# Kernel optimization log

Hardware: AMD Instinct MI355X
Metric: run time of the kernel (lower is better)

Reference implementation:

```python
import math
import jax, jax.numpy as jnp
import numpy as np

B, M, L, H = 8, 2048, 2048, 1024


def setup_inputs() -> dict:
    key = jax.random.key(0)
    k1, k2, k3, k4 = jax.random.split(key, 4)
    return {
        "query": jax.random.normal(k1, (B, M, H), dtype=jnp.float32),
        "key": jax.random.normal(k2, (B, L, H), dtype=jnp.float32),
        "value": jax.random.normal(k3, (B, L, H), dtype=jnp.float32),
        "key_pe": jax.random.normal(k4, (1, H, L), dtype=jnp.float32),
        "hidden_size": H,
    }


def reference(query, key, value, key_pe, hidden_size):
    # content scores: [B, M, L]
    attn_cont = jnp.einsum("bmh,blh->bml", query, key)
    # relative-position scores: [B, M, H] @ [1, H, L] -> [B, M, L]
    attn_pos = jnp.matmul(query, key_pe)
    # NOTE: the original module computes softmax(attn)+dropout but then
    # (as written) multiplies VALUE by the raw content scores, not the
    # softmaxed attention. We reproduce that math faithfully; the softmax
    # is dead code w.r.t. the output (kept here for documentation, DCE'd by jit).
    attn = jax.nn.softmax((attn_cont + attn_pos) / math.sqrt(hidden_size), axis=-1)  # noqa: F841
    # dropout: identity in eval mode (and unused for the output anyway)
    out = jnp.matmul(attn_cont, value)  # [B, M, H]
    return out
```

## Files before the change

kernel.cpp:

```cpp
#include <hip/hip_runtime.h>
#include <hip/hip_bf16.h>


typedef __bf16 bf16x8 __attribute__((ext_vector_type(8)));
typedef float f32x4 __attribute__((ext_vector_type(4)));
typedef unsigned short u16_t;

#define GLD_LDS16(g, l)                                                        \
  __builtin_amdgcn_global_load_lds(                                            \
      (const __attribute__((address_space(1))) void*)(g),                      \
      (__attribute__((address_space(3))) void*)(l), 16, 0, 0)

static __device__ inline u16_t f2b(float x) {
  __hip_bfloat16 h = __float2bfloat16(x);
  u16_t u;
  __builtin_memcpy(&u, &h, 2);
  return u;
}
static __device__ inline unsigned pack2(float a, float b) {
  return (unsigned)f2b(a) | ((unsigned)f2b(b) << 16);
}
static __device__ inline float b2f(u16_t u) {
  unsigned v = (unsigned)u << 16;
  float f;
  __builtin_memcpy(&f, &v, 4);
  return f;
}

__global__ __launch_bounds__(256) void transpose_kv(
    const float* __restrict__ Kin, const float* __restrict__ Vin,
    u16_t* __restrict__ Kt, u16_t* __restrict__ Vt, int L, int Hd, int ldT) {
  __shared__ unsigned tile[64][260];
  const int bz = blockIdx.z;
  const float* in = (bz < 8) ? Kin : Vin;
  u16_t* out = (bz < 8) ? Kt : Vt;
  const int batch = bz & 7;
  in += (size_t)batch * (size_t)L * Hd;
  out += (size_t)batch * (size_t)Hd * ldT;
  const int h0 = blockIdx.x * 64;
  const int l0 = blockIdx.y * 512;

  const int tid = threadIdx.x;
  const int h4 = (tid & 15) * 4;
  const int lp0 = tid >> 4;

#pragma unroll
  for (int g = 0; g < 4; ++g) {
    float4 r0[4], r1[4];
#pragma unroll
    for (int it = 0; it < 4; ++it) {
      const int lp = lp0 + 16 * (4 * g + it);
      const int l = l0 + 2 * lp;
      r0[it] = *(const float4*)(in + (size_t)l * Hd + h0 + h4);
      r1[it] = *(const float4*)(in + (size_t)(l + 1) * Hd + h0 + h4);
    }
#pragma unroll
    for (int it = 0; it < 4; ++it) {
      const int lp = lp0 + 16 * (4 * g + it);
      tile[h4 + 0][lp] = pack2(r0[it].x, r1[it].x);
      tile[h4 + 1][lp] = pack2(r0[it].y, r1[it].y);
      tile[h4 + 2][lp] = pack2(r0[it].z, r1[it].z);
      tile[h4 + 3][lp] = pack2(r0[it].w, r1[it].w);
    }
  }
  __syncthreads();

  const int wv = tid >> 6;
  const int lane = tid & 63;
#pragma unroll
  for (int r = 0; r < 16; ++r) {
    const int h = wv * 16 + r;
    unsigned u[4];
#pragma unroll
    for (int j = 0; j < 4; ++j) u[j] = tile[h][4 * lane + j];
    *(uint4*)(out + (size_t)(h0 + h) * ldT + l0 + lane * 8) = *(const uint4*)u;
  }
}

static __device__ inline void store_c(float* p, float v) { *p = v; }
static __device__ inline void store_c(u16_t* p, float v) { *p = f2b(v); }

template <typename OutT>
static __device__ inline void gemm_bt_body(
    const u16_t* __restrict__ A, const u16_t* __restrict__ Bt,
    OutT* __restrict__ C, int N, int K, int ldA, int ldB,
    long sA, long sB, long sC, int tile_shift, long sCsplit) {
  __shared__ __align__(16) u16_t As[128 * 64];
  __shared__ __align__(16) u16_t Bs[128 * 64];

  const int batch = blockIdx.x & 7;
  const unsigned u = blockIdx.x >> 3;
  const int kh = (int)(u >> tile_shift);
  const unsigned t = u & ((1u << tile_shift) - 1u);
  const int m0 = (int)(t >> 3) * 128;
  const int n0 = (int)(t & 7) * 128;

  A  += (size_t)batch * (size_t)sA + (size_t)kh * (size_t)K;
  Bt += (size_t)batch * (size_t)sB + (size_t)kh * (size_t)K;
  C  += (size_t)batch * (size_t)sC + (size_t)kh * (size_t)sCsplit;

  const int tid = threadIdx.x;
  const int lane = tid & 63;
  const int w  = tid >> 6;
  const int wm = w & 1;
  const int wn = w >> 1;
  const int s  = lane & 15;
  const int q  = lane >> 4;

  const u16_t* gA[4];
  const u16_t* gB[4];
  u16_t* lA[4];
  u16_t* lB[4];
#pragma unroll
  for (int j = 0; j < 4; ++j) {
    const int i = tid + 256 * j;
    const int row = i >> 3;
    const int gchunk = (i & 7) ^ (row & 7);
    gA[j] = A  + (size_t)(m0 + row) * ldA + gchunk * 8;
    gB[j] = Bt + (size_t)(n0 + row) * ldB + gchunk * 8;
    lA[j] = As + i * 8;
    lB[j] = Bs + i * 8;
  }

  f32x4 acc[4][4];
#pragma unroll
  for (int r = 0; r < 4; ++r)
#pragma unroll
    for (int c = 0; c < 4; ++c) acc[r][c] = (f32x4){0.f, 0.f, 0.f, 0.f};

  const int s7 = s & 7;

  for (int k0 = 0; k0 < K; k0 += 64) {
#pragma unroll
    for (int j = 0; j < 4; ++j) {
      GLD_LDS16(gA[j] + k0, lA[j]);
      GLD_LDS16(gB[j] + k0, lB[j]);
    }
    __syncthreads();

#pragma unroll
    for (int kk = 0; kk < 2; ++kk) {
      const int slot = (kk * 4 + q) ^ s7;
      bf16x8 af[4], bfr[4];
#pragma unroll
      for (int r = 0; r < 4; ++r)
        af[r] = *(const bf16x8*)(As + (64 * wm + 16 * r + s) * 64 + slot * 8);
#pragma unroll
      for (int c = 0; c < 4; ++c)
        bfr[c] = *(const bf16x8*)(Bs + (64 * wn + 16 * c + s) * 64 + slot * 8);
#pragma unroll
      for (int r = 0; r < 4; ++r)
#pragma unroll
        for (int c = 0; c < 4; ++c)
          acc[r][c] = __builtin_amdgcn_mfma_f32_16x16x32_bf16(af[r], bfr[c],
                                                              acc[r][c], 0, 0, 0);
    }
    __syncthreads();
  }

#pragma unroll
  for (int r = 0; r < 4; ++r) {
#pragma unroll
    for (int c = 0; c < 4; ++c) {
      const int col = n0 + 64 * wn + 16 * c + s;
#pragma unroll
      for (int e = 0; e < 4; ++e) {
        const int row = m0 + 64 * wm + 16 * r + q * 4 + e;
        store_c(&C[(size_t)row * N + col], acc[r][c][e]);
      }
    }
  }
}

__global__ __launch_bounds__(256) void gemm1_kv(
    const u16_t* __restrict__ Vt, const u16_t* __restrict__ Kt,
    u16_t* __restrict__ W0, int N, int K, int ld, long sA, long sB, long sC,
    long sCsplit) {
  gemm_bt_body<u16_t>(Vt, Kt, W0, N, K, ld, ld, sA, sB, sC, 6, sCsplit);
}

__global__ __launch_bounds__(256) void gemm2_qw(
    const u16_t* __restrict__ Qb, const u16_t* __restrict__ Wb,
    float* __restrict__ C, int N, int K, long sA, long sB, long sC) {
  gemm_bt_body<float>(Qb, Wb, C, N, K, K, K, sA, sB, sC, 7, 0);
}

__global__ __launch_bounds__(256) void qcvt_wsum(
    const float* __restrict__ Q, const u16_t* __restrict__ W0,
    const u16_t* __restrict__ W1, u16_t* __restrict__ Qb,
    u16_t* __restrict__ Wb, size_t nQbatch, size_t nWbatch) {
  const int batch = blockIdx.y;
  if (blockIdx.z == 0) {
    const size_t base = (size_t)batch * nWbatch +
                        (size_t)blockIdx.x * 2048 + threadIdx.x * 8;
    const uint4 u0 = *(const uint4*)(W0 + base);
    const uint4 u1 = *(const uint4*)(W1 + base);
    const u16_t* p0 = (const u16_t*)&u0;
    const u16_t* p1 = (const u16_t*)&u1;
    u16_t o[8];
#pragma unroll
    for (int j = 0; j < 8; ++j) o[j] = f2b(b2f(p0[j]) + b2f(p1[j]));
    *(uint4*)(Wb + base) = *(const uint4*)o;
  } else {
    const size_t base = (size_t)batch * nQbatch +
                        (size_t)blockIdx.x * 4096 + threadIdx.x * 16;
    const float* src = Q + base;
    u16_t* dst = Qb + base;
#pragma unroll
    for (int half = 0; half < 2; ++half) {
      const float4 a = *(const float4*)(src + half * 8);
      const float4 b = *(const float4*)(src + half * 8 + 4);
      unsigned o[4] = {pack2(a.x, a.y), pack2(a.z, a.w),
                       pack2(b.x, b.y), pack2(b.z, b.w)};
      *(uint4*)(dst + half * 8) = *(const uint4*)o;
    }
  }
}

extern "C" void kernel_launch(void* const* d_in, const int* in_sizes, int n_in,
                              void* d_out, int out_size, void* d_ws, size_t ws_size,
                              hipStream_t stream) {
  const int B = 8, M = 2048, L = 2048, H = 1024;
  const int ldT = L + 16;

  const float* q = (const float*)d_in[0];
  const float* k = (const float*)d_in[1];
  const float* v = (const float*)d_in[2];

  const size_t nKtP = (size_t)B * H * ldT;
  const size_t nW   = (size_t)B * H * H;
  const size_t nQ   = (size_t)B * M * H;
  const size_t need = (2 * nKtP + 2 * nW) * sizeof(u16_t);
  if (ws_size < need) return;

  u16_t* Kt = (u16_t*)d_ws;
  u16_t* Vt = Kt + nKtP;
  u16_t* W0 = Vt + nKtP;
  u16_t* W1 = W0 + nW;
  u16_t* Qb = Kt;
  u16_t* Wb = Vt;
  (void)nQ;

  dim3 tb(256);

  transpose_kv<<<dim3(H / 64, L / 512, 16), tb, 0, stream>>>(k, v, Kt, Vt, L, H,
                                                             ldT);

  gemm1_kv<<<dim3(B * 64 * 2), tb, 0, stream>>>(
      Vt, Kt, W0, H, L / 2, ldT, (long)H * ldT, (long)H * ldT, (long)H * H,
      (long)B * H * H);

  qcvt_wsum<<<dim3(512, B, 2), tb, 0, stream>>>(
      q, W0, W1, Qb, Wb, (size_t)M * H, (size_t)H * H);

  gemm2_qw<<<dim3(B * 128), tb, 0, stream>>>(
      Qb, Wb, (float*)d_out, H, H, (long)M * H, (long)H * H, (long)M * H);
}
```

Before: 330.4 us.

## Enlarge GEMM tiles to 256x256 with 512 threads and double-buffered LDS

Result: faster. 308.9 us (-6.5%).

```diff
diff --git a/kernel.cpp b/kernel.cpp
--- a/kernel.cpp
+++ b/kernel.cpp
@@ -81,19 +81,19 @@
 static __device__ inline void store_c(u16_t* p, float v) { *p = f2b(v); }
 
 template <typename OutT>
-static __device__ inline void gemm_bt_body(
+static __device__ inline void gemm256_body(
     const u16_t* __restrict__ A, const u16_t* __restrict__ Bt,
     OutT* __restrict__ C, int N, int K, int ldA, int ldB,
     long sA, long sB, long sC, int tile_shift, long sCsplit) {
-  __shared__ __align__(16) u16_t As[128 * 64];
-  __shared__ __align__(16) u16_t Bs[128 * 64];
+  __shared__ __align__(16) u16_t As[2][256 * 64];
+  __shared__ __align__(16) u16_t Bs[2][256 * 64];
 
   const int batch = blockIdx.x & 7;
   const unsigned u = blockIdx.x >> 3;
   const int kh = (int)(u >> tile_shift);
   const unsigned t = u & ((1u << tile_shift) - 1u);
-  const int m0 = (int)(t >> 3) * 128;
-  const int n0 = (int)(t & 7) * 128;
+  const int m0 = (int)(t >> 2) * 256;
+  const int n0 = (int)(t & 3) * 256;
 
   A  += (size_t)batch * (size_t)sA + (size_t)kh * (size_t)K;
   Bt += (size_t)batch * (size_t)sB + (size_t)kh * (size_t)K;
@@ -106,83 +106,91 @@
   const int wn = w >> 1;
   const int s  = lane & 15;
   const int q  = lane >> 4;
+  const int s7 = s & 7;
 
   const u16_t* gA[4];
   const u16_t* gB[4];
-  u16_t* lA[4];
-  u16_t* lB[4];
+  int lofs[4];
 #pragma unroll
   for (int j = 0; j < 4; ++j) {
-    const int i = tid + 256 * j;
+    const int i = tid + 512 * j;
     const int row = i >> 3;
     const int gchunk = (i & 7) ^ (row & 7);
     gA[j] = A  + (size_t)(m0 + row) * ldA + gchunk * 8;
     gB[j] = Bt + (size_t)(n0 + row) * ldB + gchunk * 8;
-    lA[j] = As + i * 8;
-    lB[j] = Bs + i * 8;
-  }
-
-  f32x4 acc[4][4];
-#pragma unroll
-  for (int r = 0; r < 4; ++r)
+    lofs[j] = i * 8;
+  }
+
+  f32x4 acc[8][4];
+#pragma unroll
+  for (int r = 0; r < 8; ++r)
 #pragma unroll
     for (int c = 0; c < 4; ++c) acc[r][c] = (f32x4){0.f, 0.f, 0.f, 0.f};
 
-  const int s7 = s & 7;
-
-  for (int k0 = 0; k0 < K; k0 += 64) {
-#pragma unroll
-    for (int j = 0; j < 4; ++j) {
-      GLD_LDS16(gA[j] + k0, lA[j]);
-      GLD_LDS16(gB[j] + k0, lB[j]);
-    }
-    __syncthreads();
-
+  auto STAGE = [&](u16_t* dA, u16_t* dB, int k0) {
+#pragma unroll
+    for (int j = 0; j < 4; ++j) GLD_LDS16(gA[j] + k0, dA + lofs[j]);
+#pragma unroll
+    for (int j = 0; j < 4; ++j) GLD_LDS16(gB[j] + k0, dB + lofs[j]);
+  };
+
+  auto COMPUTE = [&](const u16_t* As_, const u16_t* Bs_) {
 #pragma unroll
     for (int kk = 0; kk < 2; ++kk) {
       const int slot = (kk * 4 + q) ^ s7;
-      bf16x8 af[4], bfr[4];
-#pragma unroll
-      for (int r = 0; r < 4; ++r)
-        af[r] = *(const bf16x8*)(As + (64 * wm + 16 * r + s) * 64 + slot * 8);
+      bf16x8 bfr[4];
 #pragma unroll
       for (int c = 0; c < 4; ++c)
-        bfr[c] = *(const bf16x8*)(Bs + (64 * wn + 16 * c + s) * 64 + slot * 8);
-#pragma unroll
-      for (int r = 0; r < 4; ++r)
+        bfr[c] = *(const bf16x8*)(Bs_ + (64 * wn + 16 * c + s) * 64 + slot * 8);
+#pragma unroll
+      for (int r = 0; r < 8; ++r) {
+        const bf16x8 af =
+            *(const bf16x8*)(As_ + (128 * wm + 16 * r + s) * 64 + slot * 8);
 #pragma unroll
         for (int c = 0; c < 4; ++c)
-          acc[r][c] = __builtin_amdgcn_mfma_f32_16x16x32_bf16(af[r], bfr[c],
+          acc[r][c] = __builtin_amdgcn_mfma_f32_16x16x32_bf16(af, bfr[c],
                                                               acc[r][c], 0, 0, 0);
-    }
+      }
+    }
+  };
+
+  const int nt = K / 64;
+  STAGE(As[0], Bs[0], 0);
+  __syncthreads();
+  for (int tt = 0; tt < nt; tt += 2) {
+    if (tt + 1 < nt) STAGE(As[1], Bs[1], (tt + 1) * 64);
+    COMPUTE(As[0], Bs[0]);
     __syncthreads();
-  }
-
-#pragma unroll
-  for (int r = 0; r < 4; ++r) {
+    if (tt + 2 < nt) STAGE(As[0], Bs[0], (tt + 2) * 64);
+    COMPUTE(As[1], Bs[1]);
+    __syncthreads();
+  }
+
+#pragma unroll
+  for (int r = 0; r < 8; ++r) {
 #pragma unroll
     for (int c = 0; c < 4; ++c) {
       const int col = n0 + 64 * wn + 16 * c + s;
 #pragma unroll
       for (int e = 0; e < 4; ++e) {
-        const int row = m0 + 64 * wm + 16 * r + q * 4 + e;
+        const int row = m0 + 128 * wm + 16 * r + q * 4 + e;
         store_c(&C[(size_t)row * N + col], acc[r][c][e]);
       }
     }
   }
 }
 
-__global__ __launch_bounds__(256) void gemm1_kv(
+__global__ __launch_bounds__(512) void gemm1_kv(
     const u16_t* __restrict__ Vt, const u16_t* __restrict__ Kt,
     u16_t* __restrict__ W0, int N, int K, int ld, long sA, long sB, long sC,
     long sCsplit) {
-  gemm_bt_body<u16_t>(Vt, Kt, W0, N, K, ld, ld, sA, sB, sC, 6, sCsplit);
-}
-
-__global__ __launch_bounds__(256) void gemm2_qw(
+  gemm256_body<u16_t>(Vt, Kt, W0, N, K, ld, ld, sA, sB, sC, 4, sCsplit);
+}
+
+__global__ __launch_bounds__(512) void gemm2_qw(
     const u16_t* __restrict__ Qb, const u16_t* __restrict__ Wb,
     float* __restrict__ C, int N, int K, long sA, long sB, long sC) {
-  gemm_bt_body<float>(Qb, Wb, C, N, K, K, K, sA, sB, sC, 7, 0);
+  gemm256_body<float>(Qb, Wb, C, N, K, K, K, sA, sB, sC, 5, 0);
 }
 
 __global__ __launch_bounds__(256) void qcvt_wsum(
@@ -229,7 +237,6 @@
 
   const size_t nKtP = (size_t)B * H * ldT;
   const size_t nW   = (size_t)B * H * H;
-  const size_t nQ   = (size_t)B * M * H;
   const size_t need = (2 * nKtP + 2 * nW) * sizeof(u16_t);
   if (ws_size < need) return;
 
@@ -239,20 +246,17 @@
   u16_t* W1 = W0 + nW;
   u16_t* Qb = Kt;
   u16_t* Wb = Vt;
-  (void)nQ;
-
-  dim3 tb(256);
-
-  transpose_kv<<<dim3(H / 64, L / 512, 16), tb, 0, stream>>>(k, v, Kt, Vt, L, H,
-                                                             ldT);
-
-  gemm1_kv<<<dim3(B * 64 * 2), tb, 0, stream>>>(
+
+  transpose_kv<<<dim3(H / 64, L / 512, 16), dim3(256), 0, stream>>>(
+      k, v, Kt, Vt, L, H, ldT);
+
+  gemm1_kv<<<dim3(B * 16 * 2), dim3(512), 0, stream>>>(
       Vt, Kt, W0, H, L / 2, ldT, (long)H * ldT, (long)H * ldT, (long)H * H,
       (long)B * H * H);
 
-  qcvt_wsum<<<dim3(512, B, 2), tb, 0, stream>>>(
+  qcvt_wsum<<<dim3(512, B, 2), dim3(256), 0, stream>>>(
       q, W0, W1, Qb, Wb, (size_t)M * H, (size_t)H * H);
 
-  gemm2_qw<<<dim3(B * 128), tb, 0, stream>>>(
+  gemm2_qw<<<dim3(B * 32), dim3(512), 0, stream>>>(
       Qb, Wb, (float*)d_out, H, H, (long)M * H, (long)H * H, (long)M * H);
 }
```
